# Kernel tuning notes

Measured on AMD Instinct MI355X. Metric: run time of the kernel, lower is better.

Reference implementation:

```python
import jax, jax.numpy as jnp
import numpy as np

N, E = 100000, 1600000
IN_C, OUT_C, HEADS = 128, 32, 4
NEG_SLOPE = 0.2


def setup_inputs() -> dict:
    key = jax.random.key(0)
    k1, k2, k3, k4, k5, k6 = jax.random.split(key, 6)
    x = jax.random.normal(k1, (N, IN_C), dtype=jnp.float32)
    edge_index = jax.random.randint(k2, (2, E), 0, N, dtype=jnp.int64)
    glorot = (6.0 / (IN_C + HEADS * OUT_C)) ** 0.5
    W = jax.random.uniform(k3, (IN_C, HEADS * OUT_C), jnp.float32, -glorot, glorot)
    ga = (6.0 / (1 + OUT_C)) ** 0.5
    att_src = jax.random.uniform(k4, (HEADS, OUT_C), jnp.float32, -ga, ga)
    att_dst = jax.random.uniform(k5, (HEADS, OUT_C), jnp.float32, -ga, ga)
    bias = jnp.zeros((HEADS * OUT_C,), jnp.float32)
    return {"x": x, "edge_index": edge_index, "W": W, "att_src": att_src, "att_dst": att_dst, "bias": bias}


def reference(x, edge_index, W, att_src, att_dst, bias):
    n = x.shape[0]
    # linear transform per head: [N, H, C]
    xh = (x @ W).reshape(n, HEADS, OUT_C)
    # per-node attention logits (PyG computes these per node, gathers per edge)
    a_src = jnp.einsum('nhc,hc->nh', xh, att_src)  # [N, H]
    a_dst = jnp.einsum('nhc,hc->nh', xh, att_dst)  # [N, H]
    # add self-loops (PyG default add_self_loops=True)
    loop = jnp.arange(n, dtype=edge_index.dtype)
    src = jnp.concatenate([edge_index[0], loop])
    dst = jnp.concatenate([edge_index[1], loop])
    # attention scores per edge
    e = jax.nn.leaky_relu(a_src[src] + a_dst[dst], NEG_SLOPE)  # [E+N, H]
    # scatter-softmax over destination nodes
    m = jax.ops.segment_max(e, dst, num_segments=n)
    ex = jnp.exp(e - m[dst])
    s = jax.ops.segment_sum(ex, dst, num_segments=n)
    alpha = ex / s[dst]  # [E+N, H]
    # weighted aggregation of source features
    msg = xh[src] * alpha[:, :, None]  # [E+N, H, C]
    out = jax.ops.segment_sum(msg, dst, num_segments=n)
    out = out.reshape(n, HEADS * OUT_C) + bias
    return jax.nn.relu(out)
```

## Files before the change

kernel.cpp:

```cpp
#include <hip/hip_runtime.h>

#define IN_C   128
#define HC     128
#define HEADS  4
#define NEG    0.2f

#define BSH    8
#define KMAX   512
#define EPB    4096
#define CAP    5120

#define WT_STRIDE 136

typedef __attribute__((ext_vector_type(8))) short short8;
typedef __attribute__((ext_vector_type(4))) float f32x4;

__device__ __forceinline__ uint bf16_rne(float f) {
    uint u = __float_as_uint(f);
    return (u + 0x7FFFu + ((u >> 16) & 1u)) >> 16;
}
__device__ __forceinline__ uint pack_bf2(float even, float odd) {
    return bf16_rne(even) | (bf16_rne(odd) << 16);
}
__device__ __forceinline__ float bf_lo(uint u) { return __uint_as_float(u << 16); }
__device__ __forceinline__ float bf_hi(uint u) { return __uint_as_float(u & 0xFFFF0000u); }

__global__ __launch_bounds__(256) void wprep_kernel(
    const float* __restrict__ W, ushort* __restrict__ wtb,
    int* __restrict__ bcount)
{
    const int idx = blockIdx.x * 256 + threadIdx.x;
    if (idx < KMAX) bcount[idx] = 0;
    if (idx >= 128 * WT_STRIDE) return;
    const int col = idx / WT_STRIDE;
    const int k   = idx - col * WT_STRIDE;
    wtb[idx] = (k < 128) ? (ushort)bf16_rne(W[k * HC + col]) : (ushort)0;
}

__global__ __launch_bounds__(512) void gemm_mfma_kernel(
    const float* __restrict__ x, const ushort* __restrict__ wtb,
    const float* __restrict__ att_src, const float* __restrict__ att_dst,
    ushort* __restrict__ xhb16, float* __restrict__ asrc, float* __restrict__ adst,
    int n)
{
    __shared__ __align__(16) ushort Wt[128 * WT_STRIDE];
    const int tid = threadIdx.x;
    for (int i = tid; i < 128 * WT_STRIDE / 2; i += 512)
        ((uint*)Wt)[i] = ((const uint*)wtb)[i];
    __syncthreads();

    const int lane = tid & 63;
    const int wid  = tid >> 6;
    const int l15  = lane & 15;
    const int lk   = lane >> 4;
    const int row0 = blockIdx.x * 128 + wid * 16;
    const uint arow = (uint)min(row0 + l15, n - 1);
    f32x4 acc[8];
#pragma unroll
    for (int ct = 0; ct < 8; ++ct) acc[ct] = (f32x4){0.f, 0.f, 0.f, 0.f};

#pragma unroll
    for (int kc = 0; kc < 4; ++kc) {
        const uint koff = kc * 32 + lk * 8;
        const float4 fa = *(const float4*)&x[arow * 128u + koff];
        const float4 fb = *(const float4*)&x[arow * 128u + koff + 4u];
        uint4 av = make_uint4(pack_bf2(fa.x, fa.y), pack_bf2(fa.z, fa.w),
                              pack_bf2(fb.x, fb.y), pack_bf2(fb.z, fb.w));
        const short8 afrag = *(short8*)&av;
#pragma unroll
        for (int ct = 0; ct < 8; ++ct) {
            const int col = ct * 16 + l15;
            const short8 bfrag = *(const short8*)&Wt[col * WT_STRIDE + koff];
            acc[ct] = __builtin_amdgcn_mfma_f32_16x16x32_bf16(
                afrag, bfrag, acc[ct], 0, 0, 0);
        }
    }

    float as_lo[4], as_hi[4], ad_lo[4], ad_hi[4];
#pragma unroll
    for (int h = 0; h < 4; ++h) {
        as_lo[h] = att_src[h * 32 + l15];
        as_hi[h] = att_src[h * 32 + 16 + l15];
        ad_lo[h] = att_dst[h * 32 + l15];
        ad_hi[h] = att_dst[h * 32 + 16 + l15];
    }

#pragma unroll
    for (int reg = 0; reg < 4; ++reg) {
        const int r = row0 + lk * 4 + reg;
        const bool ok = r < n;
        if (ok) {
#pragma unroll
            for (int ct = 0; ct < 8; ++ct)
                xhb16[(uint)r * 128u + ct * 16 + l15] =
                    (ushort)bf16_rne(acc[ct][reg]);
        }
        float p0 = acc[0][reg] * as_lo[0] + acc[1][reg] * as_hi[0];
        float p1 = acc[2][reg] * as_lo[1] + acc[3][reg] * as_hi[1];
        float p2 = acc[4][reg] * as_lo[2] + acc[5][reg] * as_hi[2];
        float p3 = acc[6][reg] * as_lo[3] + acc[7][reg] * as_hi[3];
        float q0 = acc[0][reg] * ad_lo[0] + acc[1][reg] * ad_hi[0];
        float q1 = acc[2][reg] * ad_lo[1] + acc[3][reg] * ad_hi[1];
        float q2 = acc[4][reg] * ad_lo[2] + acc[5][reg] * ad_hi[2];
        float q3 = acc[6][reg] * ad_lo[3] + acc[7][reg] * ad_hi[3];
#pragma unroll
        for (int m = 1; m < 16; m <<= 1) {
            p0 += __shfl_xor(p0, m); p1 += __shfl_xor(p1, m);
            p2 += __shfl_xor(p2, m); p3 += __shfl_xor(p3, m);
            q0 += __shfl_xor(q0, m); q1 += __shfl_xor(q1, m);
            q2 += __shfl_xor(q2, m); q3 += __shfl_xor(q3, m);
        }
        if (l15 == 0 && ok) {
            *(float4*)&asrc[(uint)r * 4u] = make_float4(p0, p1, p2, p3);
            *(float4*)&adst[(uint)r * 4u] = make_float4(q0, q1, q2, q3);
        }
    }
}

__global__ __launch_bounds__(256) void p1_partition_kernel(
    const int* __restrict__ src, const int* __restrict__ dst,
    int* __restrict__ bcount, uint* __restrict__ staged, int E)
{
    __shared__ int  hist[KMAX];
    __shared__ int  lbase[KMAX];
    __shared__ int  gbase[KMAX];
    __shared__ int  lcur[KMAX];
    __shared__ int  sd[256];
    __shared__ uint2 stage[EPB];
    const int t = threadIdx.x;
    hist[t] = 0; hist[t + 256] = 0;
    __syncthreads();

    const int base = blockIdx.x * EPB;
    uint sv[EPB / 256], dv[EPB / 256];
#pragma unroll
    for (int i = 0; i < EPB / 256; ++i) {
        const int e = base + i * 256 + t;
        if (e < E) {
            sv[i] = (uint)src[e];
            dv[i] = (uint)dst[e];
            atomicAdd(&hist[dv[i] >> BSH], 1);
        } else {
            dv[i] = 0xFFFFFFFFu;
        }
    }
    __syncthreads();

    const int h0 = hist[2 * t], h1 = hist[2 * t + 1];
    sd[t] = h0 + h1;
    __syncthreads();
#pragma unroll
    for (int off = 1; off < 256; off <<= 1) {
        const int v = (t >= off) ? sd[t - off] : 0;
        __syncthreads();
        sd[t] += v;
        __syncthreads();
    }
    const int b2 = t ? sd[t - 1] : 0;
    lbase[2 * t]     = b2;      lcur[2 * t]     = b2;
    lbase[2 * t + 1] = b2 + h0; lcur[2 * t + 1] = b2 + h0;
    gbase[2 * t]     = h0 ? (2 * t) * CAP + atomicAdd(&bcount[2 * t], h0) : 0;
    gbase[2 * t + 1] = h1 ? (2 * t + 1) * CAP + atomicAdd(&bcount[2 * t + 1], h1) : 0;
    __syncthreads();

#pragma unroll
    for (int i = 0; i < EPB / 256; ++i) {
        if (dv[i] != 0xFFFFFFFFu) {
            const int slot = atomicAdd(&lcur[dv[i] >> BSH], 1);
            stage[slot] = make_uint2(sv[i], dv[i]);
        }
    }
    __syncthreads();

    const int total = sd[255];
    for (int j = t; j < total; j += 256) {
        const uint2 ev = stage[j];
        const int b = ev.y >> BSH;
        staged[gbase[b] + (j - lbase[b])] = ((ev.y & 255u) << 24) | ev.x;
    }
}

__global__ __launch_bounds__(256) void p2_csr_kernel(
    const uint* __restrict__ staged, const int* __restrict__ bcount,
    int* __restrict__ csr_src, int* __restrict__ node_beg,
    int* __restrict__ deg_out, int n)
{
    __shared__ int deg[256];
    __shared__ int cur[256];
    __shared__ int sd[256];
    __shared__ int sorted[CAP];
    const int b  = blockIdx.x;
    const int t  = threadIdx.x;
    const int eb = b * CAP;
    const int cnt = min(bcount[b], CAP);
    const int v0 = b << BSH;

    deg[t] = 0;
    __syncthreads();

    uint val[CAP / 256];
#pragma unroll
    for (int j = 0; j < CAP / 256; ++j) {
        const int i = j * 256 + t;
        val[j] = (i < cnt) ? staged[eb + i] : 0xFFFFFFFFu;
        if (val[j] != 0xFFFFFFFFu) atomicAdd(&deg[val[j] >> 24], 1);
    }
    __syncthreads();

    const int d = deg[t];
    sd[t] = d;
    __syncthreads();
#pragma unroll
    for (int off = 1; off < 256; off <<= 1) {
        const int v = (t >= off) ? sd[t - off] : 0;
        __syncthreads();
        sd[t] += v;
        __syncthreads();
    }
    const int excl = t ? sd[t - 1] : 0;
    cur[t] = excl;
    if (v0 + t < n) {
        node_beg[v0 + t] = eb + excl;
        deg_out[v0 + t]  = d;
    }
    __syncthreads();

#pragma unroll
    for (int j = 0; j < CAP / 256; ++j) {
        if (val[j] != 0xFFFFFFFFu) {
            const int slot = atomicAdd(&cur[val[j] >> 24], 1);
            sorted[slot] = (int)(val[j] & 0x00FFFFFFu);
        }
    }
    __syncthreads();

    for (int i = t; i < cnt; i += 256)
        csr_src[eb + i] = sorted[i];
}

__global__ __launch_bounds__(256) void aggregate_csr_kernel(
    const int* __restrict__ csr_src, const int* __restrict__ node_beg,
    const int* __restrict__ deg,
    const float* __restrict__ asrc, const float* __restrict__ adst,
    const uint* __restrict__ xhb, const float* __restrict__ bias,
    float* __restrict__ out, int n)
{
    const int node = blockIdx.x * 4 + (threadIdx.x >> 6);
    if (node >= n) return;
    const int  lane = threadIdx.x & 63;
    const int  sub  = lane >> 4;
    const uint l16  = lane & 15;
    const uint h    = l16 >> 2;
    const uint coff = l16 * 4u;

    const int beg = node_beg[node];
    const int end = beg + deg[node];

    const float adh = adst[(uint)node * 4u + h];

    const float zs = asrc[(uint)node * 4u + h] + adh;
    const float ws = (sub == 0) ? __expf(fmaxf(zs, NEG * zs)) : 0.f;
    const uint4 xs = *(const uint4*)&xhb[(uint)node * 64u + coff];
    float acc[8];
    acc[0] = ws * bf_lo(xs.x); acc[1] = ws * bf_hi(xs.x);
    acc[2] = ws * bf_lo(xs.y); acc[3] = ws * bf_hi(xs.y);
    acc[4] = ws * bf_lo(xs.z); acc[5] = ws * bf_hi(xs.z);
    acc[6] = ws * bf_lo(xs.w); acc[7] = ws * bf_hi(xs.w);
    float ssum = ws;

    if (beg < end) {
        int  eg0 = beg + sub;
        bool v0  = eg0 < end;
        uint s0  = v0 ? (uint)csr_src[eg0] : (uint)node;
        float a0 = asrc[s0 * 4u + h];
        uint4 x0 = *(const uint4*)&xhb[s0 * 64u + coff];

        for (int e = beg; e < end; e += 4) {
            const int  eg1 = e + 4 + sub;
            const bool v1  = eg1 < end;
            const uint s1  = v1 ? (uint)csr_src[eg1] : (uint)node;
            const float a1 = asrc[s1 * 4u + h];
            const uint4 x1 = *(const uint4*)&xhb[s1 * 64u + coff];

            const float z = a0 + adh;
            float w = __expf(fmaxf(z, NEG * z));
            w = v0 ? w : 0.f;
            acc[0] = fmaf(w, bf_lo(x0.x), acc[0]);
            acc[1] = fmaf(w, bf_hi(x0.x), acc[1]);
            acc[2] = fmaf(w, bf_lo(x0.y), acc[2]);
            acc[3] = fmaf(w, bf_hi(x0.y), acc[3]);
            acc[4] = fmaf(w, bf_lo(x0.z), acc[4]);
            acc[5] = fmaf(w, bf_hi(x0.z), acc[5]);
            acc[6] = fmaf(w, bf_lo(x0.w), acc[6]);
            acc[7] = fmaf(w, bf_hi(x0.w), acc[7]);
            ssum += w;

            v0 = v1; a0 = a1; x0 = x1;
        }
    }

    ssum += __shfl_xor(ssum, 16);
    ssum += __shfl_xor(ssum, 32);
#pragma unroll
    for (int j = 0; j < 8; ++j) {
        acc[j] += __shfl_xor(acc[j], 16);
        acc[j] += __shfl_xor(acc[j], 32);
    }

    if (sub == 0) {
        const float inv = 1.f / ssum;
        const uint  c   = l16 * 8u;
        const float4 b0 = *(const float4*)&bias[c];
        const float4 b1 = *(const float4*)&bias[c + 4];
        float4 o0, o1;
        o0.x = fmaf(acc[0], inv, b0.x); o0.y = fmaf(acc[1], inv, b0.y);
        o0.z = fmaf(acc[2], inv, b0.z); o0.w = fmaf(acc[3], inv, b0.w);
        o1.x = fmaf(acc[4], inv, b1.x); o1.y = fmaf(acc[5], inv, b1.y);
        o1.z = fmaf(acc[6], inv, b1.z); o1.w = fmaf(acc[7], inv, b1.w);
        o0.x = fmaxf(o0.x, 0.f); o0.y = fmaxf(o0.y, 0.f);
        o0.z = fmaxf(o0.z, 0.f); o0.w = fmaxf(o0.w, 0.f);
        o1.x = fmaxf(o1.x, 0.f); o1.y = fmaxf(o1.y, 0.f);
        o1.z = fmaxf(o1.z, 0.f); o1.w = fmaxf(o1.w, 0.f);
        *(float4*)&out[(uint)node * 128u + c]      = o0;
        *(float4*)&out[(uint)node * 128u + c + 4u] = o1;
    }
}

extern "C" void kernel_launch(void* const* d_in, const int* in_sizes, int n_in,
                              void* d_out, int out_size, void* d_ws, size_t ws_size,
                              hipStream_t stream)
{
    const float* x       = (const float*)d_in[0];
    const int*   ei      = (const int*)d_in[1];
    const float* W       = (const float*)d_in[2];
    const float* att_src = (const float*)d_in[3];
    const float* att_dst = (const float*)d_in[4];
    const float* bias    = (const float*)d_in[5];

    const int n = in_sizes[0] / IN_C;
    const int E = in_sizes[1] / 2;
    const int* src = ei;
    const int* dst = ei + E;

    float* out = (float*)d_out;

    uint*  xhb       = (uint*)d_ws;
    float* asrc      = (float*)(xhb + (size_t)n * 64);
    float* adst      = asrc + (size_t)n * HEADS;
    int*   node_beg  = (int*)(adst + (size_t)n * HEADS);
    int*   deg       = node_beg + n;
    int*   bcount    = deg + n;
    uint*  staged    = (uint*)(bcount + 512);
    int*   csr_src   = (int*)(staged + (size_t)KMAX * CAP);
    ushort* wtb      = (ushort*)(csr_src + (size_t)KMAX * CAP);

    const int K   = (n + 255) >> BSH;
    const int NB  = (E + EPB - 1) / EPB;

    wprep_kernel<<<(128 * WT_STRIDE + 255) / 256, 256, 0, stream>>>(W, wtb, bcount);
    gemm_mfma_kernel<<<(n + 127) / 128, 512, 0, stream>>>(
        x, wtb, att_src, att_dst, (ushort*)xhb, asrc, adst, n);
    p1_partition_kernel<<<NB, 256, 0, stream>>>(src, dst, bcount, staged, E);
    p2_csr_kernel<<<K, 256, 0, stream>>>(staged, bcount,
                                         csr_src, node_beg, deg, n);
    aggregate_csr_kernel<<<(n + 3) / 4, 256, 0, stream>>>(csr_src, node_beg, deg,
                                                          asrc, adst, xhb, bias,
                                                          out, n);
}
```

Before: 151.9 us.

## Fuse GEMM and edge-partition kernels into one interleaved launch

Merges the MFMA feature GEMM and the edge bucket-partition pass into one kernel. Blocks alternate between the two roles so the compute-bound GEMM and the memory/atomic-bound partition can overlap on the device, and one launch is removed. The partition path now uses 512 threads, 2048-edge tiles and a 512-wide scan. That doubles the number of partition blocks and global bucket atomics, and every block reserves the larger shared-memory footprint.

Measured after the change: 140.6 us, median of 2. 7.4% less time.

```diff
diff --git a/kernel.cpp b/kernel.cpp
--- a/kernel.cpp
+++ b/kernel.cpp
@@ -7,7 +7,7 @@
 
 #define BSH    8
 #define KMAX   512
-#define EPB    4096
+#define EPB_F  2048
 #define CAP    5120
 
 #define WT_STRIDE 136
@@ -37,146 +37,158 @@
     wtb[idx] = (k < 128) ? (ushort)bf16_rne(W[k * HC + col]) : (ushort)0;
 }
 
-__global__ __launch_bounds__(512) void gemm_mfma_kernel(
+__global__ __launch_bounds__(512) void fused_gemm_p1_kernel(
     const float* __restrict__ x, const ushort* __restrict__ wtb,
     const float* __restrict__ att_src, const float* __restrict__ att_dst,
     ushort* __restrict__ xhb16, float* __restrict__ asrc, float* __restrict__ adst,
-    int n)
-{
-    __shared__ __align__(16) ushort Wt[128 * WT_STRIDE];
+    const int* __restrict__ src, const int* __restrict__ dst,
+    int* __restrict__ bcount, uint* __restrict__ staged,
+    int n, int E)
+{
+    __shared__ __align__(16) char smem[128 * WT_STRIDE * 2];
+
+    const int G = (n + 127) >> 7;
+    const int P = (E + EPB_F - 1) / EPB_F;
+    const int M = min(G, P);
+    const int b = blockIdx.x;
+    bool is_p1;
+    int  idx;
+    if (b < 2 * M) { is_p1 = (b & 1);  idx = b >> 1; }
+    else           { is_p1 = (P > G);  idx = M + (b - 2 * M); }
+
     const int tid = threadIdx.x;
-    for (int i = tid; i < 128 * WT_STRIDE / 2; i += 512)
-        ((uint*)Wt)[i] = ((const uint*)wtb)[i];
-    __syncthreads();
-
-    const int lane = tid & 63;
-    const int wid  = tid >> 6;
-    const int l15  = lane & 15;
-    const int lk   = lane >> 4;
-    const int row0 = blockIdx.x * 128 + wid * 16;
-    const uint arow = (uint)min(row0 + l15, n - 1);
-    f32x4 acc[8];
-#pragma unroll
-    for (int ct = 0; ct < 8; ++ct) acc[ct] = (f32x4){0.f, 0.f, 0.f, 0.f};
-
-#pragma unroll
-    for (int kc = 0; kc < 4; ++kc) {
-        const uint koff = kc * 32 + lk * 8;
-        const float4 fa = *(const float4*)&x[arow * 128u + koff];
-        const float4 fb = *(const float4*)&x[arow * 128u + koff + 4u];
-        uint4 av = make_uint4(pack_bf2(fa.x, fa.y), pack_bf2(fa.z, fa.w),
-                              pack_bf2(fb.x, fb.y), pack_bf2(fb.z, fb.w));
-        const short8 afrag = *(short8*)&av;
-#pragma unroll
-        for (int ct = 0; ct < 8; ++ct) {
-            const int col = ct * 16 + l15;
-            const short8 bfrag = *(const short8*)&Wt[col * WT_STRIDE + koff];
-            acc[ct] = __builtin_amdgcn_mfma_f32_16x16x32_bf16(
-                afrag, bfrag, acc[ct], 0, 0, 0);
-        }
-    }
-
-    float as_lo[4], as_hi[4], ad_lo[4], ad_hi[4];
-#pragma unroll
-    for (int h = 0; h < 4; ++h) {
-        as_lo[h] = att_src[h * 32 + l15];
-        as_hi[h] = att_src[h * 32 + 16 + l15];
-        ad_lo[h] = att_dst[h * 32 + l15];
-        ad_hi[h] = att_dst[h * 32 + 16 + l15];
-    }
-
-#pragma unroll
-    for (int reg = 0; reg < 4; ++reg) {
-        const int r = row0 + lk * 4 + reg;
-        const bool ok = r < n;
-        if (ok) {
-#pragma unroll
-            for (int ct = 0; ct < 8; ++ct)
-                xhb16[(uint)r * 128u + ct * 16 + l15] =
-                    (ushort)bf16_rne(acc[ct][reg]);
-        }
-        float p0 = acc[0][reg] * as_lo[0] + acc[1][reg] * as_hi[0];
-        float p1 = acc[2][reg] * as_lo[1] + acc[3][reg] * as_hi[1];
-        float p2 = acc[4][reg] * as_lo[2] + acc[5][reg] * as_hi[2];
-        float p3 = acc[6][reg] * as_lo[3] + acc[7][reg] * as_hi[3];
-        float q0 = acc[0][reg] * ad_lo[0] + acc[1][reg] * ad_hi[0];
-        float q1 = acc[2][reg] * ad_lo[1] + acc[3][reg] * ad_hi[1];
-        float q2 = acc[4][reg] * ad_lo[2] + acc[5][reg] * ad_hi[2];
-        float q3 = acc[6][reg] * ad_lo[3] + acc[7][reg] * ad_hi[3];
-#pragma unroll
-        for (int m = 1; m < 16; m <<= 1) {
-            p0 += __shfl_xor(p0, m); p1 += __shfl_xor(p1, m);
-            p2 += __shfl_xor(p2, m); p3 += __shfl_xor(p3, m);
-            q0 += __shfl_xor(q0, m); q1 += __shfl_xor(q1, m);
-            q2 += __shfl_xor(q2, m); q3 += __shfl_xor(q3, m);
-        }
-        if (l15 == 0 && ok) {
-            *(float4*)&asrc[(uint)r * 4u] = make_float4(p0, p1, p2, p3);
-            *(float4*)&adst[(uint)r * 4u] = make_float4(q0, q1, q2, q3);
-        }
-    }
-}
-
-__global__ __launch_bounds__(256) void p1_partition_kernel(
-    const int* __restrict__ src, const int* __restrict__ dst,
-    int* __restrict__ bcount, uint* __restrict__ staged, int E)
-{
-    __shared__ int  hist[KMAX];
-    __shared__ int  lbase[KMAX];
-    __shared__ int  gbase[KMAX];
-    __shared__ int  lcur[KMAX];
-    __shared__ int  sd[256];
-    __shared__ uint2 stage[EPB];
-    const int t = threadIdx.x;
-    hist[t] = 0; hist[t + 256] = 0;
-    __syncthreads();
-
-    const int base = blockIdx.x * EPB;
-    uint sv[EPB / 256], dv[EPB / 256];
-#pragma unroll
-    for (int i = 0; i < EPB / 256; ++i) {
-        const int e = base + i * 256 + t;
-        if (e < E) {
-            sv[i] = (uint)src[e];
-            dv[i] = (uint)dst[e];
-            atomicAdd(&hist[dv[i] >> BSH], 1);
-        } else {
-            dv[i] = 0xFFFFFFFFu;
-        }
-    }
-    __syncthreads();
-
-    const int h0 = hist[2 * t], h1 = hist[2 * t + 1];
-    sd[t] = h0 + h1;
-    __syncthreads();
-#pragma unroll
-    for (int off = 1; off < 256; off <<= 1) {
-        const int v = (t >= off) ? sd[t - off] : 0;
-        __syncthreads();
-        sd[t] += v;
-        __syncthreads();
-    }
-    const int b2 = t ? sd[t - 1] : 0;
-    lbase[2 * t]     = b2;      lcur[2 * t]     = b2;
-    lbase[2 * t + 1] = b2 + h0; lcur[2 * t + 1] = b2 + h0;
-    gbase[2 * t]     = h0 ? (2 * t) * CAP + atomicAdd(&bcount[2 * t], h0) : 0;
-    gbase[2 * t + 1] = h1 ? (2 * t + 1) * CAP + atomicAdd(&bcount[2 * t + 1], h1) : 0;
-    __syncthreads();
-
-#pragma unroll
-    for (int i = 0; i < EPB / 256; ++i) {
-        if (dv[i] != 0xFFFFFFFFu) {
-            const int slot = atomicAdd(&lcur[dv[i] >> BSH], 1);
-            stage[slot] = make_uint2(sv[i], dv[i]);
-        }
-    }
-    __syncthreads();
-
-    const int total = sd[255];
-    for (int j = t; j < total; j += 256) {
-        const uint2 ev = stage[j];
-        const int b = ev.y >> BSH;
-        staged[gbase[b] + (j - lbase[b])] = ((ev.y & 255u) << 24) | ev.x;
+
+    if (!is_p1) {
+        ushort* Wt = (ushort*)smem;
+        for (int i = tid; i < 128 * WT_STRIDE / 2; i += 512)
+            ((uint*)Wt)[i] = ((const uint*)wtb)[i];
+        __syncthreads();
+
+        const int lane = tid & 63;
+        const int wid  = tid >> 6;
+        const int l15  = lane & 15;
+        const int lk   = lane >> 4;
+        const int row0 = idx * 128 + wid * 16;
+        const uint arow = (uint)min(row0 + l15, n - 1);
+
+        f32x4 acc[8];
+#pragma unroll
+        for (int ct = 0; ct < 8; ++ct) acc[ct] = (f32x4){0.f, 0.f, 0.f, 0.f};
+
+#pragma unroll
+        for (int kc = 0; kc < 4; ++kc) {
+            const uint koff = kc * 32 + lk * 8;
+            const float4 fa = *(const float4*)&x[arow * 128u + koff];
+            const float4 fb = *(const float4*)&x[arow * 128u + koff + 4u];
+            uint4 av = make_uint4(pack_bf2(fa.x, fa.y), pack_bf2(fa.z, fa.w),
+                                  pack_bf2(fb.x, fb.y), pack_bf2(fb.z, fb.w));
+            const short8 afrag = *(short8*)&av;
+#pragma unroll
+            for (int ct = 0; ct < 8; ++ct) {
+                const int col = ct * 16 + l15;
+                const short8 bfrag = *(const short8*)&Wt[col * WT_STRIDE + koff];
+                acc[ct] = __builtin_amdgcn_mfma_f32_16x16x32_bf16(
+                    afrag, bfrag, acc[ct], 0, 0, 0);
+            }
+        }
+
+        float as_lo[4], as_hi[4], ad_lo[4], ad_hi[4];
+#pragma unroll
+        for (int h = 0; h < 4; ++h) {
+            as_lo[h] = att_src[h * 32 + l15];
+            as_hi[h] = att_src[h * 32 + 16 + l15];
+            ad_lo[h] = att_dst[h * 32 + l15];
+            ad_hi[h] = att_dst[h * 32 + 16 + l15];
+        }
+
+#pragma unroll
+        for (int reg = 0; reg < 4; ++reg) {
+            const int r = row0 + lk * 4 + reg;
+            const bool ok = r < n;
+            if (ok) {
+#pragma unroll
+                for (int ct = 0; ct < 8; ++ct)
+                    xhb16[(uint)r * 128u + ct * 16 + l15] =
+                        (ushort)bf16_rne(acc[ct][reg]);
+            }
+            float p0 = acc[0][reg] * as_lo[0] + acc[1][reg] * as_hi[0];
+            float p1 = acc[2][reg] * as_lo[1] + acc[3][reg] * as_hi[1];
+            float p2 = acc[4][reg] * as_lo[2] + acc[5][reg] * as_hi[2];
+            float p3 = acc[6][reg] * as_lo[3] + acc[7][reg] * as_hi[3];
+            float q0 = acc[0][reg] * ad_lo[0] + acc[1][reg] * ad_hi[0];
+            float q1 = acc[2][reg] * ad_lo[1] + acc[3][reg] * ad_hi[1];
+            float q2 = acc[4][reg] * ad_lo[2] + acc[5][reg] * ad_hi[2];
+            float q3 = acc[6][reg] * ad_lo[3] + acc[7][reg] * ad_hi[3];
+#pragma unroll
+            for (int m = 1; m < 16; m <<= 1) {
+                p0 += __shfl_xor(p0, m); p1 += __shfl_xor(p1, m);
+                p2 += __shfl_xor(p2, m); p3 += __shfl_xor(p3, m);
+                q0 += __shfl_xor(q0, m); q1 += __shfl_xor(q1, m);
+                q2 += __shfl_xor(q2, m); q3 += __shfl_xor(q3, m);
+            }
+            if (l15 == 0 && ok) {
+                *(float4*)&asrc[(uint)r * 4u] = make_float4(p0, p1, p2, p3);
+                *(float4*)&adst[(uint)r * 4u] = make_float4(q0, q1, q2, q3);
+            }
+        }
+    } else {
+        int*   hist  = (int*)smem;
+        int*   lbase = hist  + KMAX;
+        int*   gbase = lbase + KMAX;
+        int*   lcur  = gbase + KMAX;
+        int*   sd    = lcur  + KMAX;
+        uint2* stage = (uint2*)(sd + KMAX);
+
+        const int t = tid;
+        hist[t] = 0;
+        __syncthreads();
+
+        const int base = idx * EPB_F;
+        uint sv[EPB_F / 512], dv[EPB_F / 512];
+#pragma unroll
+        for (int i = 0; i < EPB_F / 512; ++i) {
+            const int e = base + i * 512 + t;
+            if (e < E) {
+                sv[i] = (uint)src[e];
+                dv[i] = (uint)dst[e];
+                atomicAdd(&hist[dv[i] >> BSH], 1);
+            } else {
+                dv[i] = 0xFFFFFFFFu;
+            }
+        }
+        __syncthreads();
+
+        const int h0 = hist[t];
+        sd[t] = h0;
+        __syncthreads();
+#pragma unroll
+        for (int off = 1; off < 512; off <<= 1) {
+            const int v = (t >= off) ? sd[t - off] : 0;
+            __syncthreads();
+            sd[t] += v;
+            __syncthreads();
+        }
+        const int excl = t ? sd[t - 1] : 0;
+        lbase[t] = excl;
+        lcur[t]  = excl;
+        gbase[t] = h0 ? t * CAP + atomicAdd(&bcount[t], h0) : 0;
+        __syncthreads();
+
+#pragma unroll
+        for (int i = 0; i < EPB_F / 512; ++i) {
+            if (dv[i] != 0xFFFFFFFFu) {
+                const int slot = atomicAdd(&lcur[dv[i] >> BSH], 1);
+                stage[slot] = make_uint2(sv[i], dv[i]);
+            }
+        }
+        __syncthreads();
+
+        const int total = sd[KMAX - 1];
+        for (int j = t; j < total; j += 512) {
+            const uint2 ev = stage[j];
+            const int bb = ev.y >> BSH;
+            staged[gbase[bb] + (j - lbase[bb])] = ((ev.y & 255u) << 24) | ev.x;
+        }
     }
 }
 
@@ -354,13 +366,14 @@
     int*   csr_src   = (int*)(staged + (size_t)KMAX * CAP);
     ushort* wtb      = (ushort*)(csr_src + (size_t)KMAX * CAP);
 
-    const int K   = (n + 255) >> BSH;
-    const int NB  = (E + EPB - 1) / EPB;
+    const int K  = (n + 255) >> BSH;
+    const int G  = (n + 127) >> 7;
+    const int P  = (E + EPB_F - 1) / EPB_F;
 
     wprep_kernel<<<(128 * WT_STRIDE + 255) / 256, 256, 0, stream>>>(W, wtb, bcount);
-    gemm_mfma_kernel<<<(n + 127) / 128, 512, 0, stream>>>(
-        x, wtb, att_src, att_dst, (ushort*)xhb, asrc, adst, n);
-    p1_partition_kernel<<<NB, 256, 0, stream>>>(src, dst, bcount, staged, E);
+    fused_gemm_p1_kernel<<<G + P, 512, 0, stream>>>(
+        x, wtb, att_src, att_dst, (ushort*)xhb, asrc, adst,
+        src, dst, bcount, staged, n, E);
     p2_csr_kernel<<<K, 256, 0, stream>>>(staged, bcount,
                                          csr_src, node_beg, deg, n);
     aggregate_csr_kernel<<<(n + 3) / 4, 256, 0, stream>>>(csr_src, node_beg, deg,
```
